# Kernel optimization log

Measured on AMD Instinct MI355X. Metric: run time of the kernel, lower is better.

Reference implementation:

```python
import jax, jax.numpy as jnp
import numpy as np
from math import factorial as fact

L_MAX = 3
K = 128
N = 8192

# ---- Clebsch-Gordan coefficients (Racah formula, real for integer l) ----

def _cg_coeff(l1, m1, l2, m2, l3, m3):
    if m1 + m2 != m3:
        return 0.0
    pref = ((2 * l3 + 1) * fact(l3 + l1 - l2) * fact(l3 - l1 + l2)
            * fact(l1 + l2 - l3) / fact(l1 + l2 + l3 + 1)) ** 0.5
    pref *= (fact(l3 + m3) * fact(l3 - m3) * fact(l1 - m1) * fact(l1 + m1)
             * fact(l2 - m2) * fact(l2 + m2)) ** 0.5
    s = 0.0
    for k in range(max(0, l2 - l3 - m1, l1 - l3 + m2),
                   min(l1 + l2 - l3, l1 - m1, l2 + m2) + 1):
        s += (-1) ** k / (fact(k) * fact(l1 + l2 - l3 - k) * fact(l1 - m1 - k)
                          * fact(l2 + m2 - k) * fact(l3 - l2 + m1 + k)
                          * fact(l3 - l1 - m2 + k))
    return pref * s


def _cg_tensor(l1, l2, l3):
    C = np.zeros((2 * l1 + 1, 2 * l2 + 1, 2 * l3 + 1), dtype=np.float32)
    for m1 in range(-l1, l1 + 1):
        for m2 in range(-l2, l2 + 1):
            m3 = m1 + m2
            if -l3 <= m3 <= l3:
                C[m1 + l1, m2 + l2, m3 + l3] = _cg_coeff(l1, m1, l2, m2, l3, m3)
    return jnp.asarray(C)

# all allowed (l1, l2, l3) coupling paths, deterministic order
PATHS = [(l1, l2, l3)
         for l1 in range(L_MAX + 1)
         for l2 in range(L_MAX + 1)
         for l3 in range(abs(l1 - l2), min(l1 + l2, L_MAX) + 1)]
CG = {p: _cg_tensor(*p) for p in PATHS}
N_PATHS = [sum(1 for p in PATHS if p[2] == l3) for l3 in range(L_MAX + 1)]  # [4,9,11,10]


def setup_inputs() -> dict:
    key = jax.random.key(0)
    ks = jax.random.split(key, 12)
    inp = {}
    for i, l in enumerate(range(L_MAX + 1)):
        inp[f"f1_l{l}"] = jax.random.normal(ks[i], (N, 2 * l + 1, K), jnp.float32)
        inp[f"f2_l{l}"] = jax.random.normal(ks[4 + i], (N, 2 * l + 1, K), jnp.float32)
        fan_in = N_PATHS[l] * K
        inp[f"W_l{l}"] = jax.random.normal(ks[8 + i], (fan_in, K), jnp.float32) / np.sqrt(fan_in)
    return inp


def _forward(f1, f2, W):
    # CG tensor product: per-path contraction, channel-wise in k
    tp = [[] for _ in range(L_MAX + 1)]
    for (l1, l2, l3) in PATHS:
        C = CG[(l1, l2, l3)]  # [2l1+1, 2l2+1, 2l3+1]
        tp[l3].append(jnp.einsum('abm,nak,nbk->nmk', C, f1[l1], f2[l2]))
    # concat paths along channels, linear mix back to K, residual add
    outs = []
    for l3 in range(L_MAX + 1):
        cat = jnp.concatenate(tp[l3], axis=-1)        # [N, 2l3+1, n_paths*K]
        mixed = jnp.einsum('nmp,pk->nmk', cat, W[l3])  # [N, 2l3+1, K]
        outs.append(f1[l3] + mixed)
    return tuple(outs)


def reference(f1_l0, f1_l1, f1_l2, f1_l3,
              f2_l0, f2_l1, f2_l2, f2_l3,
              W_l0, W_l1, W_l2, W_l3):
    f1 = [f1_l0, f1_l1, f1_l2, f1_l3]
    f2 = [f2_l0, f2_l1, f2_l2, f2_l3]
    W = [W_l0, W_l1, W_l2, W_l3]
    return _forward(f1, f2, W)
```

## Files before the change

### kernel.cpp

```cpp
#include <hip/hip_runtime.h>

#define K_DIM 128

typedef __attribute__((ext_vector_type(8))) short short8;
typedef __attribute__((ext_vector_type(4))) float f32x4;

constexpr int C_L1[34] = {0,0,0,0, 1,1,1,1,1,1,1,1,1, 2,2,2,2,2,2,2,2,2,2,2, 3,3,3,3,3,3,3,3,3,3};
constexpr int C_L2[34] = {0,1,2,3, 0,1,1,1,2,2,2,3,3, 0,1,1,1,2,2,2,2,3,3,3, 0,1,1,2,2,2,3,3,3,3};
constexpr int C_L3[34] = {0,1,2,3, 1,0,1,2,1,2,3,2,3, 2,1,2,3,0,1,2,3,1,2,3, 3,2,3,1,2,3,0,1,2,3};
constexpr int C_NP[4]  = {4,9,11,10};
constexpr int C_PL[4][11] = {
  {0,5,17,30, 0,0,0,0,0,0,0},
  {1,4,6,8,14,18,21,27,31, 0,0},
  {2,7,9,11,13,15,19,22,25,28,32},
  {3,10,12,16,20,23,24,26,29,33, 0}
};
constexpr int C_CSUM[4] = {0,8,26,48};
constexpr size_t FOFF[4] = {0, 1048576, 4194304, 9437184};
constexpr int FSZ[4] = {1048576, 3145728, 5242880, 7340032};
constexpr size_t FTOT = 16777216;

__device__ double dfactd(int n){ double r=1.0; for(int i=2;i<=n;++i) r*=(double)i; return r; }

__device__ __forceinline__ unsigned short f2bf(float x) {
    unsigned int b = __float_as_uint(x);
    return (unsigned short)((b + 0x7FFFu + ((b >> 16) & 1u)) >> 16);
}
__device__ __forceinline__ float bflo(unsigned int u){ return __uint_as_float(u << 16); }
__device__ __forceinline__ float bfhi(unsigned int u){ return __uint_as_float(u & 0xFFFF0000u); }

__device__ __forceinline__ unsigned int cvtpk(float lo, float hi) {
    unsigned int r;
    asm("v_cvt_pk_bf16_f32 %0, %1, %2" : "=v"(r) : "v"(lo), "v"(hi));
    return r;
}

__global__ void cg_init(float* __restrict__ C2) {
    int e = blockIdx.x*blockDim.x + threadIdx.x;
    if (e >= 34*49) return;
    int p = e/49, r = e%49, m1i = r/7, m2i = r%7;
    int l1 = C_L1[p], l2 = C_L2[p], l3 = C_L3[p];
    float val = 0.f;
    if (m1i < 2*l1+1 && m2i < 2*l2+1) {
        int m1 = m1i-l1, m2 = m2i-l2, m3 = m1+m2;
        if (m3 >= -l3 && m3 <= l3) {
            double pref = sqrt((double)(2*l3+1) * dfactd(l3+l1-l2)*dfactd(l3-l1+l2)
                               * dfactd(l1+l2-l3) / dfactd(l1+l2+l3+1));
            pref *= sqrt(dfactd(l3+m3)*dfactd(l3-m3)*dfactd(l1-m1)*dfactd(l1+m1)
                         *dfactd(l2-m2)*dfactd(l2+m2));
            int kmin = max(0, max(l2-l3-m1, l1-l3+m2));
            int kmax = min(l1+l2-l3, min(l1-m1, l2+m2));
            double s = 0.0;
            for (int k=kmin;k<=kmax;++k) {
                double t = dfactd(k)*dfactd(l1+l2-l3-k)*dfactd(l1-m1-k)
                         * dfactd(l2+m2-k)*dfactd(l3-l2+m1+k)*dfactd(l3-l1-m2+k);
                s += ((k&1)? -1.0:1.0)/t;
            }
            val = (float)(pref*s);
        }
    }
    C2[e] = val;
}

__global__ void wt_prep(const float* __restrict__ W0, const float* __restrict__ W1,
                        const float* __restrict__ W2, const float* __restrict__ W3,
                        unsigned short* __restrict__ wt) {
    int b = blockIdx.x;
    int chunk = b >> 5;
    int e = ((b & 31) << 8) + threadIdx.x;
    int kk = e & 63, col = e >> 6;
    int l3 = (chunk < 8) ? 0 : (chunk < 26) ? 1 : (chunk < 48) ? 2 : 3;
    int local = chunk - C_CSUM[l3];
    int kin = local*64 + kk;
    const float* W = (l3==0)?W0:(l3==1)?W1:(l3==2)?W2:W3;
    float v = W[(size_t)kin*K_DIM + col];
    wt[(size_t)chunk*8192 + col*64 + (kk ^ ((col&7)<<3))] = f2bf(v);
}

__global__ void fpack(const float* __restrict__ s0, const float* __restrict__ s1,
                      const float* __restrict__ s2, const float* __restrict__ s3,
                      const float* __restrict__ s4, const float* __restrict__ s5,
                      const float* __restrict__ s6, const float* __restrict__ s7,
                      unsigned short* __restrict__ dst) {
    int y = blockIdx.y;
    int l = y & 3, fi = y >> 2;
    const float* srcs[8] = {s0,s1,s2,s3,s4,s5,s6,s7};
    const float* src = srcs[y];
    int i4 = blockIdx.x*256 + threadIdx.x;
    if (i4*4 >= FSZ[l]) return;
    float4 v = reinterpret_cast<const float4*>(src)[i4];
    unsigned int u0 = (unsigned int)f2bf(v.x) | ((unsigned int)f2bf(v.y) << 16);
    unsigned int u1 = (unsigned int)f2bf(v.z) | ((unsigned int)f2bf(v.w) << 16);
    unsigned short* d = dst + fi*FTOT + FOFF[l] + (size_t)i4*4;
    *reinterpret_cast<uint2*>(d) = make_uint2(u0, u1);
}

template<int L3, int PI>
__device__ __forceinline__ void node_pair(
    const unsigned short* __restrict__ f1b, const unsigned short* __restrict__ f2b,
    const unsigned short* __restrict__ wt, const float* __restrict__ C2,
    float* C2s, unsigned char* Asb,
    int tid, int n0, int wid, int lr, int lg, f32x4 (&cacc)[2*L3+1])
{
    constexpr int P  = C_PL[L3][PI];
    constexpr int l1 = C_L1[P], l2 = C_L2[P];
    constexpr int d1 = 2*l1+1, d2 = 2*l2+1;
    constexpr int TL3 = 2*L3+1;

    if (tid < 49) C2s[tid] = C2[P*49 + tid];

    const int nodel = tid >> 5;
    const int chq   = tid & 31;

    #pragma unroll
    for (int h = 0; h < 2; ++h) {
        __syncthreads();
        const unsigned short* g1 = f1b + FOFF[l1] + (size_t)(n0+nodel)*(d1*128) + h*64 + chq*2;
        const unsigned short* g2 = f2b + FOFF[l2] + (size_t)(n0+nodel)*(d2*128) + h*64 + chq*2;
        unsigned int q1[d1], q2[d2];
        #pragma unroll
        for (int t=0;t<d1;++t) q1[t] = *reinterpret_cast<const unsigned int*>(g1 + t*128);
        #pragma unroll
        for (int t=0;t<d2;++t) q2[t] = *reinterpret_cast<const unsigned int*>(g2 + t*128);
        const unsigned char* wbase = (const unsigned char*)
            (wt + (size_t)(C_CSUM[L3] + PI*2 + h) * 8192);
        const int col = 16*wid + lr;
        const int wkey = (col&7)<<4;
        short8 wf0 = *reinterpret_cast<const short8*>(wbase + col*128 + ((16*lg     ) ^ wkey));
        short8 wf1 = *reinterpret_cast<const short8*>(wbase + col*128 + ((16*lg + 64) ^ wkey));
        float a[TL3][2];
        #pragma unroll
        for (int mt=0;mt<TL3;++mt) { a[mt][0]=0.f; a[mt][1]=0.f; }
        #pragma unroll
        for (int m2i=0; m2i<d2; ++m2i) {
            float y0 = bflo(q2[m2i]), y1 = bfhi(q2[m2i]);
            #pragma unroll
            for (int m1i=0; m1i<d1; ++m1i) {
                int mt = (m1i-l1) + (m2i-l2) + L3;
                if (mt >= 0 && mt < TL3) {
                    float c = C2s[m1i*7 + m2i];
                    a[mt][0] = fmaf(c*bflo(q1[m1i]), y0, a[mt][0]);
                    a[mt][1] = fmaf(c*bfhi(q1[m1i]), y1, a[mt][1]);
                }
            }
        }
        #pragma unroll
        for (int mt=0; mt<TL3; ++mt) {
            int row = nodel*TL3 + mt;
            *reinterpret_cast<unsigned int*>(
                Asb + row*128 + ((chq*4) ^ ((row&7)<<4))) = cvtpk(a[mt][0], a[mt][1]);
        }
        __syncthreads();
        #pragma unroll
        for (int ks=0; ks<2; ++ks) {
            #pragma unroll
            for (int rt=0; rt<TL3; ++rt) {
                int arow = 16*rt + lr;
                short8 af = *reinterpret_cast<const short8*>(
                    Asb + arow*128 + ((16*lg + 64*ks) ^ ((arow&7)<<4)));
                cacc[rt] = __builtin_amdgcn_mfma_f32_16x16x32_bf16(
                    af, ks ? wf1 : wf0, cacc[rt], 0, 0, 0);
            }
        }
    }
}

template<int L3, int PI>
__device__ __forceinline__ void node_paths(
    const unsigned short* __restrict__ f1b, const unsigned short* __restrict__ f2b,
    const unsigned short* __restrict__ wt, const float* __restrict__ C2,
    float* C2s, unsigned char* Asb,
    int tid, int n0, int wid, int lr, int lg, f32x4 (&cacc)[2*L3+1])
{
    if constexpr (PI < C_NP[L3]) {
        node_pair<L3, PI>(f1b, f2b, wt, C2, C2s, Asb, tid, n0, wid, lr, lg, cacc);
        node_paths<L3, PI+1>(f1b, f2b, wt, C2, C2s, Asb, tid, n0, wid, lr, lg, cacc);
    }
}

template<int L3>
__device__ __forceinline__ void run16(
    int n0,
    const unsigned short* __restrict__ f1b, const unsigned short* __restrict__ f2b,
    const unsigned short* __restrict__ wt, const float* __restrict__ C2,
    float* __restrict__ out, float* C2s, unsigned char* Asb)
{
    constexpr int TL3 = 2*L3+1;
    const int tid  = threadIdx.x;
    const int lane = tid & 63, wid = tid >> 6;
    const int lr   = lane & 15, lg = lane >> 4;
    constexpr size_t OB = FOFF[L3];

    f32x4 cacc[TL3];
    #pragma unroll
    for (int rt=0; rt<TL3; ++rt) cacc[rt] = (f32x4){0.f,0.f,0.f,0.f};

    node_paths<L3, 0>(f1b, f2b, wt, C2, C2s, Asb, tid, n0, wid, lr, lg, cacc);

    const unsigned short* __restrict__ fr = f1b + OB;
    const int col = 16*wid + lr;
    #pragma unroll
    for (int rt=0; rt<TL3; ++rt) {
        #pragma unroll
        for (int i=0;i<4;++i) {
            size_t ro = (size_t)(n0*TL3 + 16*rt + 4*lg + i) * K_DIM;
            float res = __uint_as_float((unsigned int)fr[ro + col] << 16);
            out[OB + ro + col] = res + cacc[rt][i];
        }
    }
}

__global__ __launch_bounds__(512, 4) void cg_main(
    const unsigned short* __restrict__ f1b, const unsigned short* __restrict__ f2b,
    const unsigned short* __restrict__ wt,
    const float* __restrict__ C2, float* __restrict__ out)
{
    __shared__ __align__(16) unsigned char Asb[14336];
    __shared__ float C2s[49];

    int bid = blockIdx.x;
    int x = bid & 7, j = bid >> 3;
    int rnd = j >> 4, k = j & 15;
    int l3 = k >> 2, q = k & 3;
    int n0 = x*1024 + rnd*64 + q*16;
    if (l3 == 0)      run16<0>(n0, f1b, f2b, wt, C2, out, C2s, Asb);
    else if (l3 == 1) run16<1>(n0, f1b, f2b, wt, C2, out, C2s, Asb);
    else if (l3 == 2) run16<2>(n0, f1b, f2b, wt, C2, out, C2s, Asb);
    else              run16<3>(n0, f1b, f2b, wt, C2, out, C2s, Asb);
}

extern "C" void kernel_launch(void* const* d_in, const int* in_sizes, int n_in,
                              void* d_out, int out_size, void* d_ws, size_t ws_size,
                              hipStream_t stream) {
    const float* f10 = (const float*)d_in[0];
    const float* f20 = (const float*)d_in[1];
    const float* W0  = (const float*)d_in[2];
    const float* f11 = (const float*)d_in[3];
    const float* f21 = (const float*)d_in[4];
    const float* W1  = (const float*)d_in[5];
    const float* f12 = (const float*)d_in[6];
    const float* f22 = (const float*)d_in[7];
    const float* W2  = (const float*)d_in[8];
    const float* f13 = (const float*)d_in[9];
    const float* f23 = (const float*)d_in[10];
    const float* W3  = (const float*)d_in[11];

    float* C2 = (float*)d_ws;
    unsigned short* wtw = (unsigned short*)((char*)d_ws + 8192);
    unsigned short* f1b = (unsigned short*)((char*)d_ws + 1122304);
    unsigned short* f2b = f1b + FTOT;
    float* out = (float*)d_out;

    hipLaunchKernelGGL(cg_init, dim3(7), dim3(256), 0, stream, C2);
    hipLaunchKernelGGL(wt_prep, dim3(68*32), dim3(256), 0, stream, W0, W1, W2, W3, wtw);
    hipLaunchKernelGGL(fpack, dim3(7168, 8), dim3(256), 0, stream,
        f10, f11, f12, f13, f20, f21, f22, f23, f1b);
    hipLaunchKernelGGL(cg_main, dim3(2048), dim3(512), 0, stream,
        f1b, f2b, wtw, C2, out);
}
```

Measured before the change: 192.6 us.

## Preload all node features into registers and restage epilogue through LDS

Each block now loads every l-degree slice of f1 and f2 for its 16 nodes into registers once, instead of reloading them per path and per half. Both channel halves are written to a doubled LDS tile, so each path needs one barrier pair rather than two, and the weight fragments for both halves are loaded up front. The epilogue stages the MFMA accumulators through LDS so that the residual read and output write use coalesced float4 accesses. The cost is much higher register pressure: launch bounds drop from 4 to 2 blocks per CU and LDS use doubles, which lowers occupancy.

```diff
diff --git a/kernel.cpp b/kernel.cpp
--- a/kernel.cpp
+++ b/kernel.cpp
@@ -96,11 +96,11 @@
 }
 
 template<int L3, int PI>
-__device__ __forceinline__ void node_pair(
-    const unsigned short* __restrict__ f1b, const unsigned short* __restrict__ f2b,
+__device__ __forceinline__ void res_path(
+    const unsigned int (&q1)[16][2], const unsigned int (&q2)[16][2],
     const unsigned short* __restrict__ wt, const float* __restrict__ C2,
     float* C2s, unsigned char* Asb,
-    int tid, int n0, int wid, int lr, int lg, f32x4 (&cacc)[2*L3+1])
+    int tid, int nodel, int chq, int wid, int lr, int lg, f32x4 (&cacc)[2*L3+1])
 {
     constexpr int P  = C_PL[L3][PI];
     constexpr int l1 = C_L1[P], l2 = C_L2[P];
@@ -108,39 +108,34 @@
     constexpr int TL3 = 2*L3+1;
 
     if (tid < 49) C2s[tid] = C2[P*49 + tid];
-
-    const int nodel = tid >> 5;
-    const int chq   = tid & 31;
-
-    #pragma unroll
-    for (int h = 0; h < 2; ++h) {
-        __syncthreads();
-        const unsigned short* g1 = f1b + FOFF[l1] + (size_t)(n0+nodel)*(d1*128) + h*64 + chq*2;
-        const unsigned short* g2 = f2b + FOFF[l2] + (size_t)(n0+nodel)*(d2*128) + h*64 + chq*2;
-        unsigned int q1[d1], q2[d2];
-        #pragma unroll
-        for (int t=0;t<d1;++t) q1[t] = *reinterpret_cast<const unsigned int*>(g1 + t*128);
-        #pragma unroll
-        for (int t=0;t<d2;++t) q2[t] = *reinterpret_cast<const unsigned int*>(g2 + t*128);
-        const unsigned char* wbase = (const unsigned char*)
-            (wt + (size_t)(C_CSUM[L3] + PI*2 + h) * 8192);
-        const int col = 16*wid + lr;
-        const int wkey = (col&7)<<4;
-        short8 wf0 = *reinterpret_cast<const short8*>(wbase + col*128 + ((16*lg     ) ^ wkey));
-        short8 wf1 = *reinterpret_cast<const short8*>(wbase + col*128 + ((16*lg + 64) ^ wkey));
+    __syncthreads();
+
+    const int col = 16*wid + lr;
+    const int wkey = (col&7)<<4;
+    const unsigned char* wb0 = (const unsigned char*)(wt + (size_t)(C_CSUM[L3] + PI*2    )*8192);
+    const unsigned char* wb1 = (const unsigned char*)(wt + (size_t)(C_CSUM[L3] + PI*2 + 1)*8192);
+    short8 wf[4];
+    wf[0] = *reinterpret_cast<const short8*>(wb0 + col*128 + ((16*lg     ) ^ wkey));
+    wf[1] = *reinterpret_cast<const short8*>(wb0 + col*128 + ((16*lg + 64) ^ wkey));
+    wf[2] = *reinterpret_cast<const short8*>(wb1 + col*128 + ((16*lg     ) ^ wkey));
+    wf[3] = *reinterpret_cast<const short8*>(wb1 + col*128 + ((16*lg + 64) ^ wkey));
+
+    #pragma unroll
+    for (int h=0; h<2; ++h) {
         float a[TL3][2];
         #pragma unroll
-        for (int mt=0;mt<TL3;++mt) { a[mt][0]=0.f; a[mt][1]=0.f; }
+        for (int mt=0; mt<TL3; ++mt) { a[mt][0]=0.f; a[mt][1]=0.f; }
         #pragma unroll
         for (int m2i=0; m2i<d2; ++m2i) {
-            float y0 = bflo(q2[m2i]), y1 = bfhi(q2[m2i]);
+            float y0 = bflo(q2[l2*l2+m2i][h]);
+            float y1 = bfhi(q2[l2*l2+m2i][h]);
             #pragma unroll
             for (int m1i=0; m1i<d1; ++m1i) {
                 int mt = (m1i-l1) + (m2i-l2) + L3;
                 if (mt >= 0 && mt < TL3) {
                     float c = C2s[m1i*7 + m2i];
-                    a[mt][0] = fmaf(c*bflo(q1[m1i]), y0, a[mt][0]);
-                    a[mt][1] = fmaf(c*bfhi(q1[m1i]), y1, a[mt][1]);
+                    a[mt][0] = fmaf(c*bflo(q1[l1*l1+m1i][h]), y0, a[mt][0]);
+                    a[mt][1] = fmaf(c*bfhi(q1[l1*l1+m1i][h]), y1, a[mt][1]);
                 }
             }
         }
@@ -148,33 +143,33 @@
         for (int mt=0; mt<TL3; ++mt) {
             int row = nodel*TL3 + mt;
             *reinterpret_cast<unsigned int*>(
-                Asb + row*128 + ((chq*4) ^ ((row&7)<<4))) = cvtpk(a[mt][0], a[mt][1]);
-        }
-        __syncthreads();
-        #pragma unroll
-        for (int ks=0; ks<2; ++ks) {
-            #pragma unroll
-            for (int rt=0; rt<TL3; ++rt) {
-                int arow = 16*rt + lr;
-                short8 af = *reinterpret_cast<const short8*>(
-                    Asb + arow*128 + ((16*lg + 64*ks) ^ ((arow&7)<<4)));
-                cacc[rt] = __builtin_amdgcn_mfma_f32_16x16x32_bf16(
-                    af, ks ? wf1 : wf0, cacc[rt], 0, 0, 0);
-            }
+                Asb + row*256 + h*128 + ((chq*4) ^ ((row&7)<<4))) = cvtpk(a[mt][0], a[mt][1]);
+        }
+    }
+    __syncthreads();
+
+    #pragma unroll
+    for (int kst=0; kst<4; ++kst) {
+        #pragma unroll
+        for (int rt=0; rt<TL3; ++rt) {
+            int arow = 16*rt + lr;
+            short8 af = *reinterpret_cast<const short8*>(
+                Asb + arow*256 + ((16*lg + 64*kst) ^ ((arow&7)<<4)));
+            cacc[rt] = __builtin_amdgcn_mfma_f32_16x16x32_bf16(af, wf[kst], cacc[rt], 0, 0, 0);
         }
     }
 }
 
 template<int L3, int PI>
-__device__ __forceinline__ void node_paths(
-    const unsigned short* __restrict__ f1b, const unsigned short* __restrict__ f2b,
+__device__ __forceinline__ void res_paths(
+    const unsigned int (&q1)[16][2], const unsigned int (&q2)[16][2],
     const unsigned short* __restrict__ wt, const float* __restrict__ C2,
     float* C2s, unsigned char* Asb,
-    int tid, int n0, int wid, int lr, int lg, f32x4 (&cacc)[2*L3+1])
+    int tid, int nodel, int chq, int wid, int lr, int lg, f32x4 (&cacc)[2*L3+1])
 {
     if constexpr (PI < C_NP[L3]) {
-        node_pair<L3, PI>(f1b, f2b, wt, C2, C2s, Asb, tid, n0, wid, lr, lg, cacc);
-        node_paths<L3, PI+1>(f1b, f2b, wt, C2, C2s, Asb, tid, n0, wid, lr, lg, cacc);
+        res_path<L3, PI>(q1, q2, wt, C2, C2s, Asb, tid, nodel, chq, wid, lr, lg, cacc);
+        res_paths<L3, PI+1>(q1, q2, wt, C2, C2s, Asb, tid, nodel, chq, wid, lr, lg, cacc);
     }
 }
 
@@ -186,36 +181,63 @@
     float* __restrict__ out, float* C2s, unsigned char* Asb)
 {
     constexpr int TL3 = 2*L3+1;
-    const int tid  = threadIdx.x;
-    const int lane = tid & 63, wid = tid >> 6;
-    const int lr   = lane & 15, lg = lane >> 4;
+    const int tid   = threadIdx.x;
+    const int nodel = tid >> 5;
+    const int chq   = tid & 31;
+    const int lane  = tid & 63, wid = tid >> 6;
+    const int lr    = lane & 15, lg = lane >> 4;
     constexpr size_t OB = FOFF[L3];
 
+    unsigned int q1[16][2], q2[16][2];
+    #pragma unroll
+    for (int l=0; l<4; ++l) {
+        const unsigned short* g1 = f1b + FOFF[l] + (size_t)(n0+nodel)*((2*l+1)*128) + chq*2;
+        const unsigned short* g2 = f2b + FOFF[l] + (size_t)(n0+nodel)*((2*l+1)*128) + chq*2;
+        #pragma unroll
+        for (int m=0; m<2*l+1; ++m) {
+            #pragma unroll
+            for (int h=0; h<2; ++h) {
+                q1[l*l+m][h] = *reinterpret_cast<const unsigned int*>(g1 + m*128 + h*64);
+                q2[l*l+m][h] = *reinterpret_cast<const unsigned int*>(g2 + m*128 + h*64);
+            }
+        }
+    }
+
     f32x4 cacc[TL3];
     #pragma unroll
     for (int rt=0; rt<TL3; ++rt) cacc[rt] = (f32x4){0.f,0.f,0.f,0.f};
 
-    node_paths<L3, 0>(f1b, f2b, wt, C2, C2s, Asb, tid, n0, wid, lr, lg, cacc);
-
+    res_paths<L3, 0>(q1, q2, wt, C2, C2s, Asb, tid, nodel, chq, wid, lr, lg, cacc);
+
+    __syncthreads();
+    float* S = reinterpret_cast<float*>(Asb);
     const unsigned short* __restrict__ fr = f1b + OB;
     const int col = 16*wid + lr;
+    const int rr = tid >> 5, c0 = (tid & 31) * 4;
     #pragma unroll
     for (int rt=0; rt<TL3; ++rt) {
         #pragma unroll
-        for (int i=0;i<4;++i) {
-            size_t ro = (size_t)(n0*TL3 + 16*rt + 4*lg + i) * K_DIM;
-            float res = __uint_as_float((unsigned int)fr[ro + col] << 16);
-            out[OB + ro + col] = res + cacc[rt][i];
-        }
-    }
-}
-
-__global__ __launch_bounds__(512, 4) void cg_main(
+        for (int i=0;i<4;++i)
+            S[(4*lg+i)*128 + col] = cacc[rt][i];
+        __syncthreads();
+        {
+            size_t ro = (size_t)(n0*TL3 + 16*rt + rr) * K_DIM;
+            float4 v = *reinterpret_cast<const float4*>(&S[rr*128 + c0]);
+            uint2 rb = *reinterpret_cast<const uint2*>(fr + ro + c0);
+            v.x += bflo(rb.x); v.y += bfhi(rb.x);
+            v.z += bflo(rb.y); v.w += bfhi(rb.y);
+            *reinterpret_cast<float4*>(&out[OB + ro + c0]) = v;
+        }
+        __syncthreads();
+    }
+}
+
+__global__ __launch_bounds__(512, 2) void cg_main(
     const unsigned short* __restrict__ f1b, const unsigned short* __restrict__ f2b,
     const unsigned short* __restrict__ wt,
     const float* __restrict__ C2, float* __restrict__ out)
 {
-    __shared__ __align__(16) unsigned char Asb[14336];
+    __shared__ __align__(16) unsigned char Asb[28672];
     __shared__ float C2s[49];
 
     int bid = blockIdx.x;
```

Result: faster. 174.1 us (-9.6%).
